# Kernel tuning notes

Measured on AMD Instinct MI355X. Metric: run time of the kernel, lower is better.

The kernel has to match this reference:

```python
import jax, jax.numpy as jnp
import numpy as np

N_EMBD = 1024
N_HEAD = 16
B, T = 4, 2048


def setup_inputs() -> dict:
    key = jax.random.key(0)
    k1, k2, k3, k4, k5 = jax.random.split(key, 5)
    s = 0.02
    return {
        "x": jax.random.normal(k1, (B, T, N_EMBD), dtype=jnp.float32),
        "w_attn": jax.random.normal(k2, (N_EMBD, 3 * N_EMBD), dtype=jnp.float32) * s,
        "b_attn": jnp.zeros((3 * N_EMBD,), dtype=jnp.float32),
        "w_proj": jax.random.normal(k3, (N_EMBD, N_EMBD), dtype=jnp.float32) * s,
        "b_proj": jnp.zeros((N_EMBD,), dtype=jnp.float32),
    }


def reference(x, w_attn, b_attn, w_proj, b_proj):
    Bb, Tt, C = x.shape
    hd = C // N_HEAD  # head dim
    qkv = x @ w_attn + b_attn                      # [B,T,3C]
    q, k, v = jnp.split(qkv, 3, axis=-1)
    # [B,T,C] -> [B,H,T,hd]
    def heads(t):
        return t.reshape(Bb, Tt, N_HEAD, hd).transpose(0, 2, 1, 3)
    q, k, v = heads(q), heads(k), heads(v)
    scale = 1.0 / np.sqrt(hd).astype(np.float32)
    attn = jnp.einsum("bhqd,bhkd->bhqk", q, k) * scale  # [B,H,T,T]
    causal = jnp.tril(jnp.ones((Tt, Tt), dtype=bool))
    attn = jnp.where(causal, attn, -jnp.inf)
    attn = jax.nn.softmax(attn, axis=-1)
    y = jnp.einsum("bhqk,bhkd->bhqd", attn, v)          # [B,H,T,hd]
    y = y.transpose(0, 2, 1, 3).reshape(Bb, Tt, C)
    return y @ w_proj + b_proj
```

## Files before the change

kernel.cpp:

```cpp
#include <hip/hip_runtime.h>
#include <cmath>


typedef short short8 __attribute__((ext_vector_type(8)));
typedef short short4v __attribute__((ext_vector_type(4)));
typedef float f32x4 __attribute__((ext_vector_type(4)));

__device__ __forceinline__ short f2bf(float f) {
  unsigned u = __builtin_bit_cast(unsigned, f);
  u = (u + 0x7fffu + ((u >> 16) & 1u)) >> 16;
  return (short)u;
}

__device__ __forceinline__ float exp2_fast(float x) {
  float r;
  asm("v_exp_f32 %0, %1" : "=v"(r) : "v"(x));
  return r;
}

__device__ __forceinline__ void gld_lds16(const void* g, void* l) {
  __builtin_amdgcn_global_load_lds(
      (__attribute__((address_space(1))) void*)g,
      (__attribute__((address_space(3))) void*)l,
      16, 0, 0);
}

__global__ void cast_bf16_kernel(const float* __restrict__ in,
                                 short* __restrict__ out, int n4) {
  int i = blockIdx.x * blockDim.x + threadIdx.x;
  if (i < n4) {
    const float4 v = ((const float4*)in)[i];
    short4v o;
    o.x = f2bf(v.x); o.y = f2bf(v.y); o.z = f2bf(v.z); o.w = f2bf(v.w);
    ((short4v*)out)[i] = o;
  }
}

__global__ void transpose_cast_kernel(const float* __restrict__ in,
                                      short* __restrict__ out, int R, int C) {
  __shared__ float tile[32][33];
  int c0 = blockIdx.x * 32, r0 = blockIdx.y * 32;
  int tx = threadIdx.x & 31, tg = threadIdx.x >> 5;
#pragma unroll
  for (int i = 0; i < 4; ++i) {
    int r = tg * 4 + i;
    tile[r][tx] = in[(size_t)(r0 + r) * C + c0 + tx];
  }
  __syncthreads();
#pragma unroll
  for (int i = 0; i < 4; ++i) {
    int c = tg * 4 + i;
    out[(size_t)(c0 + c) * R + r0 + tx] = f2bf(tile[tx][c]);
  }
}

template <int MODE>
__global__ __launch_bounds__(256) void gemm_bt_kernel(
    const short* __restrict__ A, const short* __restrict__ Bt,
    const float* __restrict__ bias, float* __restrict__ outf,
    short* __restrict__ oq, short* __restrict__ ok, short* __restrict__ ovt,
    int M, int N, int K) {
  __shared__ short As[128 * 32];
  __shared__ short Bs[128 * 32];
  const int m0 = blockIdx.y * 128, n0 = blockIdx.x * 128;
  const int lane = threadIdx.x & 63, wave = threadIdx.x >> 6;
  const int quad = lane >> 4, l16 = lane & 15;
  const int wm = (wave >> 1) * 64, wn = (wave & 1) * 64;

  const int srow = wave * 32 + (lane >> 2);
  const int scol = (lane & 3) * 8;
  const short* Ag = A + (size_t)(m0 + srow) * K + scol;
  const short* Bg = Bt + (size_t)(n0 + srow) * K + scol;
  short* AsW = &As[wave * 1024];
  short* BsW = &Bs[wave * 1024];

  f32x4 acc[4][4] = {};

  for (int k0 = 0; k0 < K; k0 += 32) {
    gld_lds16(Ag + k0, AsW);
    gld_lds16(Ag + (size_t)16 * K + k0, AsW + 512);
    gld_lds16(Bg + k0, BsW);
    gld_lds16(Bg + (size_t)16 * K + k0, BsW + 512);
    __syncthreads();
    short8 a[4], b[4];
#pragma unroll
    for (int t = 0; t < 4; ++t)
      a[t] = *(const short8*)&As[(wm + t * 16 + l16) * 32 + quad * 8];
#pragma unroll
    for (int t = 0; t < 4; ++t)
      b[t] = *(const short8*)&Bs[(wn + t * 16 + l16) * 32 + quad * 8];
#pragma unroll
    for (int mt = 0; mt < 4; ++mt)
#pragma unroll
      for (int nt = 0; nt < 4; ++nt)
        acc[mt][nt] = __builtin_amdgcn_mfma_f32_16x16x32_bf16(a[mt], b[nt],
                                                              acc[mt][nt], 0, 0, 0);
    __syncthreads();
  }

#pragma unroll
  for (int mt = 0; mt < 4; ++mt) {
#pragma unroll
    for (int nt = 0; nt < 4; ++nt) {
      const int n = n0 + wn + nt * 16 + l16;
      const float bv = bias[n];
      if (MODE == 1) {
#pragma unroll
        for (int r = 0; r < 4; ++r) {
          const int m = m0 + wm + mt * 16 + quad * 4 + r;
          outf[(size_t)m * N + n] = acc[mt][nt][r] + bv;
        }
      } else {
        const int sec = n >> 10, c = n & 1023, h = c >> 6, d = c & 63;
#pragma unroll
        for (int r = 0; r < 4; ++r) {
          const int m = m0 + wm + mt * 16 + quad * 4 + r;
          const int b_ = m >> 11, t_ = m & 2047;
          const int bh = b_ * 16 + h;
          float val = acc[mt][nt][r] + bv;
          if (sec == 0) {
            oq[((size_t)bh * 2048 + t_) * 64 + d] = f2bf(val * 0.18033688f);
          } else if (sec == 1) {
            ok[((size_t)bh * 2048 + t_) * 64 + d] = f2bf(val);
          } else {
            ovt[((size_t)bh * 64 + d) * 2048 + t_] = f2bf(val);
          }
        }
      }
    }
  }
}

__global__ __launch_bounds__(256, 6) void attn_kernel(
    const short* __restrict__ q, const short* __restrict__ k,
    const short* __restrict__ vt, short* __restrict__ y) {
  __shared__ short Ks[64 * 64];
  __shared__ short Vs[64 * 64];
  __shared__ short Ps[4][16 * 72];
  const int lane = threadIdx.x & 63, wave = threadIdx.x >> 6;
  const int quad = lane >> 4, l16 = lane & 15;
  const int g = blockIdx.x;
  const int bh = g & 63;
  const int j = 31 - (g >> 6);
  const int b_ = bh >> 4, h = bh & 15;
  const int q0 = j * 64 + wave * 16;

  const short* qbh = q + (size_t)bh * 2048 * 64;
  const short* kbh = k + (size_t)bh * 2048 * 64;
  const short* vbh = vt + (size_t)bh * 64 * 2048;
  short* Pw = Ps[wave];

  const short8 qf0 = *(const short8*)&qbh[(q0 + l16) * 64 + quad * 8];
  const short8 qf1 = *(const short8*)&qbh[(q0 + l16) * 64 + 32 + quad * 8];

  short8 ones;
#pragma unroll
  for (int i = 0; i < 8; ++i) ones[i] = (short)0x3F80;

  f32x4 O[4] = {};
  f32x4 lacc = {};

  const int srow = lane >> 3;
  const int scol = ((lane & 7) ^ srow) * 8;
  const int r0s = wave * 16;

#pragma unroll 1
  for (int c = 0; c <= j; ++c) {
    const int kt0 = c * 64;
    gld_lds16(kbh + (size_t)(kt0 + r0s + srow) * 64 + scol, &Ks[r0s * 64]);
    gld_lds16(kbh + (size_t)(kt0 + r0s + 8 + srow) * 64 + scol, &Ks[(r0s + 8) * 64]);
    gld_lds16(vbh + (size_t)(r0s + srow) * 2048 + kt0 + scol, &Vs[r0s * 64]);
    gld_lds16(vbh + (size_t)(r0s + 8 + srow) * 2048 + kt0 + scol, &Vs[(r0s + 8) * 64]);
    __syncthreads();

    const int sw = l16 & 7;
    f32x4 sc4[4];
#pragma unroll
    for (int cf = 0; cf < 4; ++cf) {
      const int row = cf * 16 + l16;
      const short8 kfa = *(const short8*)&Ks[row * 64 + ((quad ^ sw) * 8)];
      const short8 kfb = *(const short8*)&Ks[row * 64 + (((quad + 4) ^ sw) * 8)];
      f32x4 z = {};
      z = __builtin_amdgcn_mfma_f32_16x16x32_bf16(qf0, kfa, z, 0, 0, 0);
      z = __builtin_amdgcn_mfma_f32_16x16x32_bf16(qf1, kfb, z, 0, 0, 0);
      sc4[cf] = z;
    }

    if (c == j) {
#pragma unroll
      for (int cf = 0; cf < 4; ++cf) {
        const int col = kt0 + cf * 16 + l16;
#pragma unroll
        for (int r = 0; r < 4; ++r) {
          const int rowg = q0 + quad * 4 + r;
          float e = exp2_fast(sc4[cf][r]);
          e = (col > rowg) ? 0.f : e;
          Pw[(quad * 4 + r) * 72 + cf * 16 + l16] = f2bf(e);
        }
      }
    } else {
#pragma unroll
      for (int cf = 0; cf < 4; ++cf)
#pragma unroll
        for (int r = 0; r < 4; ++r)
          Pw[(quad * 4 + r) * 72 + cf * 16 + l16] = f2bf(exp2_fast(sc4[cf][r]));
    }
    asm volatile("s_waitcnt lgkmcnt(0)" ::: "memory");
    const short8 pf0 = *(const short8*)&Pw[l16 * 72 + quad * 8];
    const short8 pf1 = *(const short8*)&Pw[l16 * 72 + 32 + quad * 8];

    lacc = __builtin_amdgcn_mfma_f32_16x16x32_bf16(pf0, ones, lacc, 0, 0, 0);
    lacc = __builtin_amdgcn_mfma_f32_16x16x32_bf16(pf1, ones, lacc, 0, 0, 0);

#pragma unroll
    for (int dt = 0; dt < 4; ++dt) {
      const int d = dt * 16 + l16;
      const short8 vf0 = *(const short8*)&Vs[d * 64 + ((quad ^ sw) * 8)];
      const short8 vf1 = *(const short8*)&Vs[d * 64 + (((quad + 4) ^ sw) * 8)];
      O[dt] = __builtin_amdgcn_mfma_f32_16x16x32_bf16(pf0, vf0, O[dt], 0, 0, 0);
      O[dt] = __builtin_amdgcn_mfma_f32_16x16x32_bf16(pf1, vf1, O[dt], 0, 0, 0);
    }
    __syncthreads();
  }

  float inv[4];
#pragma unroll
  for (int r = 0; r < 4; ++r) inv[r] = 1.0f / lacc[r];
#pragma unroll
  for (int dt = 0; dt < 4; ++dt) {
    const int d = dt * 16 + l16;
#pragma unroll
    for (int r = 0; r < 4; ++r) {
      const int t_ = q0 + quad * 4 + r;
      y[((size_t)b_ * 2048 + t_) * 1024 + h * 64 + d] = f2bf(O[dt][r] * inv[r]);
    }
  }
}

extern "C" void kernel_launch(void* const* d_in, const int* in_sizes, int n_in,
                              void* d_out, int out_size, void* d_ws, size_t ws_size,
                              hipStream_t stream) {
  const float* x      = (const float*)d_in[0];
  const float* w_attn = (const float*)d_in[1];
  const float* b_attn = (const float*)d_in[2];
  const float* w_proj = (const float*)d_in[3];
  const float* b_proj = (const float*)d_in[4];
  float* out = (float*)d_out;

  short* xb  = (short*)d_ws;
  short* wTa = xb + (size_t)8192 * 1024;
  short* wTp = wTa + (size_t)3072 * 1024;
  short* qb  = wTp + (size_t)1024 * 1024;
  short* kb  = qb + (size_t)64 * 2048 * 64;
  short* vtb = kb + (size_t)64 * 2048 * 64;
  short* yb  = vtb + (size_t)64 * 2048 * 64;

  cast_bf16_kernel<<<8192, 256, 0, stream>>>(x, xb, 8192 * 1024 / 4);
  transpose_cast_kernel<<<dim3(96, 32), 256, 0, stream>>>(w_attn, wTa, 1024, 3072);
  transpose_cast_kernel<<<dim3(32, 32), 256, 0, stream>>>(w_proj, wTp, 1024, 1024);

  gemm_bt_kernel<0><<<dim3(24, 64), 256, 0, stream>>>(
      xb, wTa, b_attn, nullptr, qb, kb, vtb, 8192, 3072, 1024);

  attn_kernel<<<2048, 256, 0, stream>>>(qb, kb, vtb, yb);

  gemm_bt_kernel<1><<<dim3(8, 64), 256, 0, stream>>>(
      yb, wTp, b_proj, out, nullptr, nullptr, nullptr, 8192, 1024, 1024);
}
```

Measured before the change: 280.1 us.

## Use BK=64 with XOR-swizzled LDS and LDS-staged vectorized QKV epilogue

The GEMM main loop now loads K-tiles of 64 instead of 32, which halves the number of barrier pairs per output tile. The LDS layout uses an XOR swizzle on 16-byte segments to avoid bank conflicts on the MFMA operand reads. The QKV epilogue writes bf16 results into LDS, transposing for the V section, then issues coalesced 16-byte global stores instead of scattered 2-byte stores. LDS usage per block grows, which may reduce occupancy.

```diff
diff --git a/kernel.cpp b/kernel.cpp
--- a/kernel.cpp
+++ b/kernel.cpp
@@ -60,73 +60,102 @@
     const float* __restrict__ bias, float* __restrict__ outf,
     short* __restrict__ oq, short* __restrict__ ok, short* __restrict__ ovt,
     int M, int N, int K) {
-  __shared__ short As[128 * 32];
-  __shared__ short Bs[128 * 32];
+  __shared__ short lds[(MODE == 0) ? 17408 : 16384];
+  short* As = lds;
+  short* Bs = lds + 8192;
   const int m0 = blockIdx.y * 128, n0 = blockIdx.x * 128;
   const int lane = threadIdx.x & 63, wave = threadIdx.x >> 6;
   const int quad = lane >> 4, l16 = lane & 15;
   const int wm = (wave >> 1) * 64, wn = (wave & 1) * 64;
 
-  const int srow = wave * 32 + (lane >> 2);
-  const int scol = (lane & 3) * 8;
-  const short* Ag = A + (size_t)(m0 + srow) * K + scol;
-  const short* Bg = Bt + (size_t)(n0 + srow) * K + scol;
-  short* AsW = &As[wave * 1024];
-  short* BsW = &Bs[wave * 1024];
+  const int row_off = lane >> 3;
+  const int segsw = ((lane & 7) ^ row_off) * 8;
+  const short* Ag = A + (size_t)(m0 + wave * 32 + row_off) * K + segsw;
+  const short* Bg = Bt + (size_t)(n0 + wave * 32 + row_off) * K + segsw;
 
   f32x4 acc[4][4] = {};
 
-  for (int k0 = 0; k0 < K; k0 += 32) {
-    gld_lds16(Ag + k0, AsW);
-    gld_lds16(Ag + (size_t)16 * K + k0, AsW + 512);
-    gld_lds16(Bg + k0, BsW);
-    gld_lds16(Bg + (size_t)16 * K + k0, BsW + 512);
-    __syncthreads();
-    short8 a[4], b[4];
-#pragma unroll
-    for (int t = 0; t < 4; ++t)
-      a[t] = *(const short8*)&As[(wm + t * 16 + l16) * 32 + quad * 8];
-#pragma unroll
-    for (int t = 0; t < 4; ++t)
-      b[t] = *(const short8*)&Bs[(wn + t * 16 + l16) * 32 + quad * 8];
+  for (int k0 = 0; k0 < K; k0 += 64) {
+#pragma unroll
+    for (int g = 0; g < 4; ++g) {
+      gld_lds16(Ag + (size_t)(g * 8) * K + k0, &As[(wave * 32 + g * 8) * 64]);
+      gld_lds16(Bg + (size_t)(g * 8) * K + k0, &Bs[(wave * 32 + g * 8) * 64]);
+    }
+    __syncthreads();
+#pragma unroll
+    for (int kh = 0; kh < 2; ++kh) {
+      short8 a[4], b[4];
+#pragma unroll
+      for (int t = 0; t < 4; ++t) {
+        const int R = wm + t * 16 + l16;
+        a[t] = *(const short8*)&As[R * 64 + (((kh * 4 + quad) ^ (R & 7)) * 8)];
+      }
+#pragma unroll
+      for (int t = 0; t < 4; ++t) {
+        const int R = wn + t * 16 + l16;
+        b[t] = *(const short8*)&Bs[R * 64 + (((kh * 4 + quad) ^ (R & 7)) * 8)];
+      }
+#pragma unroll
+      for (int mt = 0; mt < 4; ++mt)
+#pragma unroll
+        for (int nt = 0; nt < 4; ++nt)
+          acc[mt][nt] = __builtin_amdgcn_mfma_f32_16x16x32_bf16(
+              a[mt], b[nt], acc[mt][nt], 0, 0, 0);
+    }
+    __syncthreads();
+  }
+
+  float bv[4];
+#pragma unroll
+  for (int nt = 0; nt < 4; ++nt) bv[nt] = bias[n0 + wn + nt * 16 + l16];
+
+  if (MODE == 1) {
 #pragma unroll
     for (int mt = 0; mt < 4; ++mt)
 #pragma unroll
-      for (int nt = 0; nt < 4; ++nt)
-        acc[mt][nt] = __builtin_amdgcn_mfma_f32_16x16x32_bf16(a[mt], b[nt],
-                                                              acc[mt][nt], 0, 0, 0);
-    __syncthreads();
-  }
-
-#pragma unroll
-  for (int mt = 0; mt < 4; ++mt) {
-#pragma unroll
-    for (int nt = 0; nt < 4; ++nt) {
-      const int n = n0 + wn + nt * 16 + l16;
-      const float bv = bias[n];
-      if (MODE == 1) {
+      for (int nt = 0; nt < 4; ++nt) {
+        const int n = n0 + wn + nt * 16 + l16;
 #pragma unroll
         for (int r = 0; r < 4; ++r) {
           const int m = m0 + wm + mt * 16 + quad * 4 + r;
-          outf[(size_t)m * N + n] = acc[mt][nt][r] + bv;
+          outf[(size_t)m * N + n] = acc[mt][nt][r] + bv[nt];
         }
-      } else {
-        const int sec = n >> 10, c = n & 1023, h = c >> 6, d = c & 63;
+      }
+  } else {
+    const int sec = n0 >> 10;
+    short* Cs = lds;
+    const float scale = (sec == 0) ? 0.18033688f : 1.0f;
+#pragma unroll
+    for (int mt = 0; mt < 4; ++mt)
+#pragma unroll
+      for (int nt = 0; nt < 4; ++nt) {
+        const int col = wn + nt * 16 + l16;
 #pragma unroll
         for (int r = 0; r < 4; ++r) {
-          const int m = m0 + wm + mt * 16 + quad * 4 + r;
-          const int b_ = m >> 11, t_ = m & 2047;
-          const int bh = b_ * 16 + h;
-          float val = acc[mt][nt][r] + bv;
-          if (sec == 0) {
-            oq[((size_t)bh * 2048 + t_) * 64 + d] = f2bf(val * 0.18033688f);
-          } else if (sec == 1) {
-            ok[((size_t)bh * 2048 + t_) * 64 + d] = f2bf(val);
-          } else {
-            ovt[((size_t)bh * 64 + d) * 2048 + t_] = f2bf(val);
-          }
+          const int row = wm + mt * 16 + quad * 4 + r;
+          const short h = f2bf((acc[mt][nt][r] + bv[nt]) * scale);
+          if (sec == 2) Cs[col * 136 + row] = h;
+          else          Cs[row * 136 + col] = h;
         }
       }
+    __syncthreads();
+
+    const int tid = threadIdx.x;
+    const int rw = tid >> 1, half = tid & 1;
+    const int h0 = (n0 & 1023) >> 6;
+    const short* sp = &Cs[rw * 136 + half * 64];
+    if (sec < 2) {
+      short* dst = (sec == 0) ? oq : ok;
+      const int m = m0 + rw, b_ = m >> 11, tt = m & 2047;
+      short* gp = dst + ((size_t)(b_ * 16 + h0 + half) * 2048 + tt) * 64;
+#pragma unroll
+      for (int i = 0; i < 8; ++i) ((short8*)gp)[i] = ((const short8*)sp)[i];
+    } else {
+      const int b_ = m0 >> 11, t0 = m0 & 2047;
+      const int bh = b_ * 16 + h0 + (rw >> 6), d = rw & 63;
+      short* gp = ovt + ((size_t)bh * 64 + d) * 2048 + t0 + half * 64;
+#pragma unroll
+      for (int i = 0; i < 8; ++i) ((short8*)gp)[i] = ((const short8*)sp)[i];
     }
   }
 }
```

Measured after the change: 263.0 us. -6.1%, faster.
